# Kernel optimization log

Hardware: AMD Instinct MI355X
Metric: run time of the kernel (lower is better)

Reference implementation:

```python
import jax, jax.numpy as jnp
import numpy as np

B, L, H = 4096, 4096, 1024  # batch, num_labels, hidden_size


def setup_inputs() -> dict:
    key = jax.random.key(0)
    k1, k2, k3, k4, k5 = jax.random.split(key, 5)
    return {
        "bert_output": jax.random.normal(k1, (B, H), dtype=jnp.float32),
        "label_embed": jax.random.normal(k2, (L, H), dtype=jnp.float32),
        "W": jax.random.normal(k3, (L, H), dtype=jnp.float32) * 0.02,
        "b": jax.random.normal(k4, (L,), dtype=jnp.float32) * 0.02,
        "labels": jax.random.randint(k5, (B, L), 0, 2, dtype=jnp.int32),
    }


def reference(bert_output, label_embed, W, b, labels):
    # Original: output[i, j] = classifier(bert_output[i] + label_embed[j])[j]
    #         = sum_k (x[i,k] + E[j,k]) * W[j,k] + b[j]
    #         = (x @ W^T)[i,j] + (E * W).sum(-1)[j] + b[j]
    xWt = jnp.einsum('bh,lh->bl', bert_output, W)          # [B, L] GEMM
    diag_bias = jnp.sum(label_embed * W, axis=-1) + b       # [L] epilogue
    logits = xWt + diag_bias[None, :]                       # [B, L]
    return logits
```

## Files before the change

kernel.cpp:

```cpp
#include <hip/hip_runtime.h>
#include <hip/hip_bf16.h>

#define Bdim 4096
#define Ldim 4096
#define Hdim 1024
#define BM 256
#define BN 256
#define BK 64
#define NT (Hdim / BK)

typedef __attribute__((ext_vector_type(8))) __bf16 bf16x8;
typedef __attribute__((ext_vector_type(4))) float floatx4;

__device__ __forceinline__ unsigned short f2bf(float f) {
  union { __hip_bfloat16 h; unsigned short u; } c;
  c.h = __float2bfloat16(f);
  return c.u;
}

__global__ __launch_bounds__(256) void prep_kernel(
    const float* __restrict__ X, const float* __restrict__ E,
    const float* __restrict__ W, const float* __restrict__ b,
    unsigned short* __restrict__ Xb, unsigned short* __restrict__ Wb,
    float* __restrict__ bias) {
  const int blk = blockIdx.x;
  const int t = threadIdx.x;
  if (blk < Ldim) {
    const int row = blk;
    const float4 wv = reinterpret_cast<const float4*>(W + (size_t)row * Hdim)[t];
    const float4 ev = reinterpret_cast<const float4*>(E + (size_t)row * Hdim)[t];
    ushort4 o;
    o.x = f2bf(wv.x); o.y = f2bf(wv.y); o.z = f2bf(wv.z); o.w = f2bf(wv.w);
    reinterpret_cast<ushort4*>(Wb + (size_t)row * Hdim)[t] = o;
    float dot = wv.x * ev.x + wv.y * ev.y + wv.z * ev.z + wv.w * ev.w;
#pragma unroll
    for (int off = 32; off > 0; off >>= 1) dot += __shfl_down(dot, off, 64);
    __shared__ float part[4];
    if ((t & 63) == 0) part[t >> 6] = dot;
    __syncthreads();
    if (t == 0) bias[row] = part[0] + part[1] + part[2] + part[3] + b[row];
  } else {
    const int i = (blk - Ldim) * 256 + t;
    float4 v = reinterpret_cast<const float4*>(X)[i];
    ushort4 o;
    o.x = f2bf(v.x); o.y = f2bf(v.y); o.z = f2bf(v.z); o.w = f2bf(v.w);
    reinterpret_cast<ushort4*>(Xb)[i] = o;
  }
}

__global__ __launch_bounds__(512, 2) void gemm_bias_kernel(
    const unsigned short* __restrict__ A,
    const unsigned short* __restrict__ Bw,
    const float* __restrict__ bias,
    float* __restrict__ C) {
  __shared__ __align__(16) unsigned short lds[2][2][BM * BK];

  const int tid = threadIdx.x;
  const int wave = tid >> 6;
  const int lane = tid & 63;
  const int wm = wave >> 2;
  const int wn = wave & 3;
  const int m_blk = blockIdx.y * BM;
  const int n_blk = blockIdx.x * BN;

  const int srow = wave * 8 + (lane >> 3);
  const int skofs = ((lane & 7) ^ (lane >> 3)) * 8;
  const unsigned short* gA = A + (size_t)(m_blk + srow) * Hdim + skofs;
  const unsigned short* gB = Bw + (size_t)(n_blk + srow) * Hdim + skofs;

  const int fr = lane & 15;
  const int fq = lane >> 4;
  const int kx0 = ((fq) ^ (fr & 7)) * 8;
  const int kx1 = ((4 + fq) ^ (fr & 7)) * 8;
  const int aBase = (wm * 128 + fr) * BK;
  const int bBase = (wn * 64 + fr) * BK;

  floatx4 acc[8][4] = {};
  bf16x8 af[8][2], bfv[4][2];

#define GLL(src, dst)                                                  \
  __builtin_amdgcn_global_load_lds(                                    \
      (const __attribute__((address_space(1))) void*)(src),            \
      (__attribute__((address_space(3))) void*)(dst), 16, 0, 0)

#define STAGE_H(c, mat, h, kt)                                         \
  do {                                                                 \
    const unsigned short* _g = (mat) ? gB : gA;                        \
    GLL(_g + (size_t)((h) * 128) * Hdim + (size_t)(kt) * BK,           \
        &lds[c][mat][((h) * 128 + wave * 8) * BK]);                    \
    GLL(_g + (size_t)((h) * 128 + 64) * Hdim + (size_t)(kt) * BK,      \
        &lds[c][mat][((h) * 128 + 64 + wave * 8) * BK]);               \
  } while (0)

#define READ_A(c, lo)                                                  \
  do {                                                                 \
    _Pragma("unroll") for (int mi = (lo); mi < (lo) + 4; ++mi) {       \
      af[mi][0] = *(const bf16x8*)&lds[c][0][aBase + mi * 16 * BK + kx0]; \
      af[mi][1] = *(const bf16x8*)&lds[c][0][aBase + mi * 16 * BK + kx1]; \
    }                                                                  \
  } while (0)

#define READ_B(c, lo)                                                  \
  do {                                                                 \
    _Pragma("unroll") for (int ni = (lo); ni < (lo) + 2; ++ni) {       \
      bfv[ni][0] = *(const bf16x8*)&lds[c][1][bBase + ni * 16 * BK + kx0]; \
      bfv[ni][1] = *(const bf16x8*)&lds[c][1][bBase + ni * 16 * BK + kx1]; \
    }                                                                  \
  } while (0)

#define MFMA_Q(M0, N0)                                                 \
  do {                                                                 \
    __builtin_amdgcn_s_setprio(1);                                     \
    _Pragma("unroll") for (int mi = (M0); mi < (M0) + 4; ++mi)         \
      _Pragma("unroll") for (int ni = (N0); ni < (N0) + 2; ++ni) {     \
        acc[mi][ni] = __builtin_amdgcn_mfma_f32_16x16x32_bf16(         \
            af[mi][0], bfv[ni][0], acc[mi][ni], 0, 0, 0);              \
        acc[mi][ni] = __builtin_amdgcn_mfma_f32_16x16x32_bf16(         \
            af[mi][1], bfv[ni][1], acc[mi][ni], 0, 0, 0);              \
      }                                                                \
    __builtin_amdgcn_s_setprio(0);                                     \
  } while (0)

#define BAR __builtin_amdgcn_s_barrier()
#define LGKM0 asm volatile("s_waitcnt lgkmcnt(0)" ::: "memory")
#define GATE4 asm volatile("s_waitcnt vmcnt(4)\n\ts_barrier" ::: "memory")
#define GATE0 asm volatile("s_waitcnt vmcnt(0)\n\ts_barrier" ::: "memory")

#define TILE_BODY(c, o, kt, DO_B, DO_A, GATE)                          \
  do {                                                                 \
                                                               \
    if (DO_B) STAGE_H(o, 1, 0, (kt) + 1);                              \
    READ_A(c, 0);                                                      \
    READ_B(c, 0);                                                      \
    BAR; LGKM0;                                                        \
    MFMA_Q(0, 0);                                                      \
                                                               \
    if (DO_B) STAGE_H(o, 1, 1, (kt) + 1);                              \
    READ_A(c, 4);                                                      \
    BAR; LGKM0;                                                        \
    MFMA_Q(4, 0);                                                      \
    BAR;   \
                                                               \
    if (DO_A) STAGE_H(c, 0, 0, (kt) + 2);                              \
    READ_B(c, 2);                                                      \
    BAR; LGKM0;                                                        \
    MFMA_Q(0, 2);                                                      \
    BAR;                  \
                                                               \
    if (DO_A) STAGE_H(c, 0, 1, (kt) + 2);                              \
    GATE;                                                              \
    MFMA_Q(4, 2);                                                      \
  } while (0)

  STAGE_H(0, 0, 0, 0);
  STAGE_H(0, 0, 1, 0);
  STAGE_H(0, 1, 0, 0);
  STAGE_H(0, 1, 1, 0);
  STAGE_H(1, 0, 0, 1);
  STAGE_H(1, 0, 1, 1);
  GATE4;

#pragma unroll 1
  for (int t = 0; t < NT - 2; t += 2) {
    TILE_BODY(0, 1, t, 1, 1, GATE4);
    TILE_BODY(1, 0, t + 1, 1, 1, GATE4);
  }
  TILE_BODY(0, 1, NT - 2, 1, 0, GATE0);
  TILE_BODY(1, 0, NT - 1, 0, 0, (void)0);

#undef GLL
#undef STAGE_H
#undef READ_A
#undef READ_B
#undef MFMA_Q
#undef BAR
#undef LGKM0
#undef GATE4
#undef GATE0
#undef TILE_BODY

  const int col0 = n_blk + wn * 64 + fr;
  const int row0 = m_blk + wm * 128 + fq * 4;
#pragma unroll
  for (int ni = 0; ni < 4; ++ni) {
    const float bs = bias[col0 + ni * 16];
#pragma unroll
    for (int mi = 0; mi < 8; ++mi) {
      float* cp = C + (size_t)(row0 + mi * 16) * Ldim + (col0 + ni * 16);
      floatx4 v = acc[mi][ni];
      cp[0 * (size_t)Ldim] = v.x + bs;
      cp[1 * (size_t)Ldim] = v.y + bs;
      cp[2 * (size_t)Ldim] = v.z + bs;
      cp[3 * (size_t)Ldim] = v.w + bs;
    }
  }
}

extern "C" void kernel_launch(void* const* d_in, const int* in_sizes, int n_in,
                              void* d_out, int out_size, void* d_ws, size_t ws_size,
                              hipStream_t stream) {
  const float* X = (const float*)d_in[0];
  const float* E = (const float*)d_in[1];
  const float* W = (const float*)d_in[2];
  const float* b = (const float*)d_in[3];
  float* out = (float*)d_out;

  unsigned short* Xb = (unsigned short*)d_ws;
  unsigned short* Wb = Xb + (size_t)Bdim * Hdim;
  float* bias = (float*)(Wb + (size_t)Ldim * Hdim);

  prep_kernel<<<Ldim + Bdim, 256, 0, stream>>>(X, E, W, b, Xb, Wb, bias);
  dim3 grid(Ldim / BN, Bdim / BM);
  gemm_bias_kernel<<<grid, 512, 0, stream>>>(Xb, Wb, bias, out);
}
```

Measured before the change: 50.23 us.

## Remap GEMM blocks per XCD, drop redundant barriers, use nontemporal memory ops

The GEMM grid is flattened to 1D and remapped so that each XCD's blocks share two rows of A tiles, which should improve L2 reuse. Several s_barrier calls inside the pipelined tile body are removed, keeping only those that guard LDS buffer overwrites, to cut synchronisation stalls between MFMA phases. The fp32 input loads in the prep kernel and the output stores in the GEMM become nontemporal to reduce cache pollution. Removing barriers risks LDS read/write races if the remaining ones do not cover every hazard.

New measurement: 59.78 us. 1.19x slower.

```diff
diff --git a/kernel.cpp b/kernel.cpp
--- a/kernel.cpp
+++ b/kernel.cpp
@@ -11,6 +11,7 @@
 
 typedef __attribute__((ext_vector_type(8))) __bf16 bf16x8;
 typedef __attribute__((ext_vector_type(4))) float floatx4;
+typedef __attribute__((ext_vector_type(4))) unsigned short ushortx4;
 
 __device__ __forceinline__ unsigned short f2bf(float f) {
   union { __hip_bfloat16 h; unsigned short u; } c;
@@ -27,11 +28,13 @@
   const int t = threadIdx.x;
   if (blk < Ldim) {
     const int row = blk;
-    const float4 wv = reinterpret_cast<const float4*>(W + (size_t)row * Hdim)[t];
-    const float4 ev = reinterpret_cast<const float4*>(E + (size_t)row * Hdim)[t];
-    ushort4 o;
+    const floatx4 wv = __builtin_nontemporal_load(
+        reinterpret_cast<const floatx4*>(W + (size_t)row * Hdim) + t);
+    const floatx4 ev = __builtin_nontemporal_load(
+        reinterpret_cast<const floatx4*>(E + (size_t)row * Hdim) + t);
+    ushortx4 o;
     o.x = f2bf(wv.x); o.y = f2bf(wv.y); o.z = f2bf(wv.z); o.w = f2bf(wv.w);
-    reinterpret_cast<ushort4*>(Wb + (size_t)row * Hdim)[t] = o;
+    reinterpret_cast<ushortx4*>(Wb + (size_t)row * Hdim)[t] = o;
     float dot = wv.x * ev.x + wv.y * ev.y + wv.z * ev.z + wv.w * ev.w;
 #pragma unroll
     for (int off = 32; off > 0; off >>= 1) dot += __shfl_down(dot, off, 64);
@@ -41,10 +44,11 @@
     if (t == 0) bias[row] = part[0] + part[1] + part[2] + part[3] + b[row];
   } else {
     const int i = (blk - Ldim) * 256 + t;
-    float4 v = reinterpret_cast<const float4*>(X)[i];
-    ushort4 o;
+    floatx4 v = __builtin_nontemporal_load(
+        reinterpret_cast<const floatx4*>(X) + i);
+    ushortx4 o;
     o.x = f2bf(v.x); o.y = f2bf(v.y); o.z = f2bf(v.z); o.w = f2bf(v.w);
-    reinterpret_cast<ushort4*>(Xb)[i] = o;
+    reinterpret_cast<ushortx4*>(Xb)[i] = o;
   }
 }
 
@@ -60,8 +64,12 @@
   const int lane = tid & 63;
   const int wm = wave >> 2;
   const int wn = wave & 3;
-  const int m_blk = blockIdx.y * BM;
-  const int n_blk = blockIdx.x * BN;
+
+  const int bid = blockIdx.x;
+  const int xcd = bid & 7;
+  const int idx = bid >> 3;
+  const int m_blk = (xcd * 2 + (idx >> 4)) * BM;
+  const int n_blk = (idx & 15) * BN;
 
   const int srow = wave * 8 + (lane >> 3);
   const int skofs = ((lane & 7) ^ (lane >> 3)) * 8;
@@ -132,23 +140,22 @@
     if (DO_B) STAGE_H(o, 1, 0, (kt) + 1);                              \
     READ_A(c, 0);                                                      \
     READ_B(c, 0);                                                      \
-    BAR; LGKM0;                                                        \
+    LGKM0;                                                             \
     MFMA_Q(0, 0);                                                      \
                                                                \
     if (DO_B) STAGE_H(o, 1, 1, (kt) + 1);                              \
     READ_A(c, 4);                                                      \
-    BAR; LGKM0;                                                        \
+    LGKM0;                                                             \
     MFMA_Q(4, 0);                                                      \
-    BAR;   \
+    BAR;  \
                                                                \
     if (DO_A) STAGE_H(c, 0, 0, (kt) + 2);                              \
     READ_B(c, 2);                                                      \
-    BAR; LGKM0;                                                        \
+    LGKM0;                                                             \
     MFMA_Q(0, 2);                                                      \
-    BAR;                  \
                                                                \
     if (DO_A) STAGE_H(c, 0, 1, (kt) + 2);                              \
-    GATE;                                                              \
+    GATE;        \
     MFMA_Q(4, 2);                                                      \
   } while (0)
 
@@ -188,10 +195,10 @@
     for (int mi = 0; mi < 8; ++mi) {
       float* cp = C + (size_t)(row0 + mi * 16) * Ldim + (col0 + ni * 16);
       floatx4 v = acc[mi][ni];
-      cp[0 * (size_t)Ldim] = v.x + bs;
-      cp[1 * (size_t)Ldim] = v.y + bs;
-      cp[2 * (size_t)Ldim] = v.z + bs;
-      cp[3 * (size_t)Ldim] = v.w + bs;
+      __builtin_nontemporal_store(v.x + bs, cp + 0 * (size_t)Ldim);
+      __builtin_nontemporal_store(v.y + bs, cp + 1 * (size_t)Ldim);
+      __builtin_nontemporal_store(v.z + bs, cp + 2 * (size_t)Ldim);
+      __builtin_nontemporal_store(v.w + bs, cp + 3 * (size_t)Ldim);
     }
   }
 }
@@ -210,6 +217,5 @@
   float* bias = (float*)(Wb + (size_t)Ldim * Hdim);
 
   prep_kernel<<<Ldim + Bdim, 256, 0, stream>>>(X, E, W, b, Xb, Wb, bias);
-  dim3 grid(Ldim / BN, Bdim / BM);
-  gemm_bias_kernel<<<grid, 512, 0, stream>>>(Xb, Wb, bias, out);
-}
+  gemm_bias_kernel<<<(Bdim / BM) * (Ldim / BN), 512, 0, stream>>>(Xb, Wb, bias, out);
+}
```
